# Kernel optimization log

Measured on AMD Instinct MI355X. Metric: run time of the kernel, lower is better.

## Reference

```python
import jax, jax.numpy as jnp
import numpy as np

DIM = 1024
N_HEAD = 16
HEAD_DIM = DIM // N_HEAD
SCALE = HEAD_DIM ** (-0.5)


def setup_inputs() -> dict:
    key = jax.random.key(0)
    ks = jax.random.split(key, 5)
    x = jax.random.normal(ks[0], (2, 2048, DIM), dtype=jnp.float32)
    # Linear params (torch nn.Linear stores weight as [out, in]; we keep [in, out])
    wqkv = jax.random.normal(ks[1], (DIM, 3 * DIM), dtype=jnp.float32) / np.sqrt(DIM)
    bqkv = jax.random.normal(ks[2], (3 * DIM,), dtype=jnp.float32) * 0.01
    wo = jax.random.normal(ks[3], (DIM, DIM), dtype=jnp.float32) / np.sqrt(DIM)
    bo = jax.random.normal(ks[4], (DIM,), dtype=jnp.float32) * 0.01
    return {"x": x, "wqkv": wqkv, "bqkv": bqkv, "wo": wo, "bo": bo}


def reference(x, wqkv, bqkv, wo, bo):
    b, s, _ = x.shape
    qkv = x @ wqkv + bqkv                      # [b, s, 3*dim]
    q, k, v = jnp.split(qkv, 3, axis=-1)
    # [b, s, h, d] -> [b, h, s, d]
    def heads(t):
        return t.reshape(b, s, N_HEAD, HEAD_DIM).transpose(0, 2, 1, 3)
    q, k, v = heads(q) * SCALE, heads(k), heads(v)
    attn = jnp.einsum('bhqd,bhkd->bhqk', q, k)  # [b, h, s, s]
    attn = jax.nn.softmax(attn, axis=-1)
    out = jnp.einsum('bhqk,bhkd->bhqd', attn, v)
    out = out.transpose(0, 2, 1, 3).reshape(b, s, DIM)
    return out @ wo + bo
```

## Files before the change

kernel.cpp:

```cpp
#include <hip/hip_runtime.h>
#include <hip/hip_bf16.h>

#define DIM   1024
#define NHEAD 16
#define HDIM  64
#define BATCH 2
#define SEQ   2048
#define TOK   (BATCH*SEQ)
#define SCALE 0.125f

typedef unsigned short u16;
typedef __attribute__((ext_vector_type(8))) short s16x8;
typedef __attribute__((ext_vector_type(4))) float f32x4;

__device__ __forceinline__ u16 f2bf(float f) {
    union { float f; unsigned u; } v; v.f = f;
    unsigned r = v.u + 0x7fffu + ((v.u >> 16) & 1u);
    return (u16)(r >> 16);
}
__device__ __forceinline__ float bf2f(u16 h) {
    union { unsigned u; float f; } v; v.u = (unsigned)h << 16;
    return v.f;
}
__device__ __forceinline__ unsigned pack2(float a, float b) {
    return (unsigned)f2bf(a) | ((unsigned)f2bf(b) << 16);
}

typedef __attribute__((address_space(3))) void lds_void;
typedef const __attribute__((address_space(1))) void gbl_void;
__device__ __forceinline__ void gload_lds16(const void* g, void* l) {
    __builtin_amdgcn_global_load_lds((gbl_void*)g, (lds_void*)l, 16, 0, 0);
}

__global__ __launch_bounds__(256)
void cvt_bf16(const float* __restrict__ in, u16* __restrict__ out) {
    int i = blockIdx.x * 256 + threadIdx.x;
    float4 v = ((const float4*)in)[i];
    ((uint2*)out)[i] = make_uint2(pack2(v.x, v.y), pack2(v.z, v.w));
}

__global__ __launch_bounds__(256)
void cvt_bf16_T(const float* __restrict__ in, u16* __restrict__ outT,
                int K, int N) {
    __shared__ float t[32][33];
    const int n0 = blockIdx.x * 32, k0 = blockIdx.y * 32;
    const int tx = threadIdx.x & 31, ty = threadIdx.x >> 5;
#pragma unroll
    for (int i = 0; i < 4; ++i)
        t[ty + i * 8][tx] = in[(size_t)(k0 + ty + i * 8) * N + n0 + tx];
    __syncthreads();
#pragma unroll
    for (int i = 0; i < 4; ++i) {
        float v = t[tx][ty + i * 8];
        outT[(size_t)(n0 + ty + i * 8) * K + k0 + tx] = f2bf(v);
    }
}

__global__ __launch_bounds__(256)
void split_cvt_T(const float* __restrict__ in, u16* __restrict__ hiT,
                 u16* __restrict__ loT, int K, int N) {
    __shared__ float t[32][33];
    const int n0 = blockIdx.x * 32, k0 = blockIdx.y * 32;
    const int tx = threadIdx.x & 31, ty = threadIdx.x >> 5;
#pragma unroll
    for (int i = 0; i < 4; ++i)
        t[ty + i * 8][tx] = in[(size_t)(k0 + ty + i * 8) * N + n0 + tx];
    __syncthreads();
#pragma unroll
    for (int i = 0; i < 4; ++i) {
        float v = t[tx][ty + i * 8];
        u16 h = f2bf(v);
        size_t o = (size_t)(n0 + ty + i * 8) * K + k0 + tx;
        hiT[o] = h;
        loT[o] = f2bf(v - bf2f(h));
    }
}

__global__ __launch_bounds__(256)
void gemm_qkv(const u16* __restrict__ Ag, const u16* __restrict__ Bg,
              const float* __restrict__ bias, u16* __restrict__ Qh,
              u16* __restrict__ Kh, u16* __restrict__ Vh, int K, int N) {
    __shared__ u16 As[128 * 64];
    __shared__ u16 Bs[128 * 64];

    const int tid  = threadIdx.x;
    const int lane = tid & 63;
    const int w    = tid >> 6;
    const int c    = lane & 15;
    const int quad = lane >> 4;
    const int wm   = (w & 1) * 64;
    const int wn   = (w >> 1) * 64;
    const int row0 = blockIdx.y * 128;
    const int col0 = blockIdx.x * 128;
    const int sw   = c & 7;

    f32x4 acc[4][4];
#pragma unroll
    for (int m = 0; m < 4; ++m)
#pragma unroll
        for (int n = 0; n < 4; ++n) acc[m][n] = (f32x4){0.f, 0.f, 0.f, 0.f};

    for (int k0 = 0; k0 < K; k0 += 64) {
        __syncthreads();
#pragma unroll
        for (int i = 0; i < 4; ++i) {
            int idx = tid + i * 256;
            int r = idx >> 3, p = idx & 7;
            int g = p ^ (r & 7);
            gload_lds16(Ag + (size_t)(row0 + r) * K + k0 + g * 8, &As[idx * 8]);
            gload_lds16(Bg + (size_t)(col0 + r) * K + k0 + g * 8, &Bs[idx * 8]);
        }
        __syncthreads();

        s16x8 af[4][2];
#pragma unroll
        for (int m = 0; m < 4; ++m)
#pragma unroll
            for (int kh = 0; kh < 2; ++kh)
                af[m][kh] = *(const s16x8*)&As[(wm + m * 16 + c) * 64 +
                                              ((kh * 4 + quad) ^ sw) * 8];
#pragma unroll
        for (int kh = 0; kh < 2; ++kh)
#pragma unroll
            for (int n = 0; n < 4; ++n) {
                s16x8 bf = *(const s16x8*)&Bs[(wn + n * 16 + c) * 64 +
                                              ((kh * 4 + quad) ^ sw) * 8];
#pragma unroll
                for (int m = 0; m < 4; ++m)
                    acc[m][n] = __builtin_amdgcn_mfma_f32_16x16x32_bf16(
                        af[m][kh], bf, acc[m][n], 0, 0, 0);
            }
    }

#pragma unroll
    for (int n = 0; n < 4; ++n) {
        const int col = col0 + wn + n * 16 + c;
        const float bv = bias[col];
        const int h = (col >> 6) & 15, d = col & 63;
#pragma unroll
        for (int m = 0; m < 4; ++m) {
            const int rbase = row0 + wm + m * 16 + quad * 4;
#pragma unroll
            for (int r = 0; r < 4; ++r) {
                const int row = rbase + r;
                const int b = row >> 11, s = row & (SEQ - 1);
                const int bh = (b << 4) + h;
                float v = acc[m][n][r] + bv;
                if (col0 < DIM)
                    Qh[((size_t)bh * SEQ + s) * 64 + d] = f2bf(v * SCALE);
                else if (col0 < 2 * DIM)
                    Kh[((size_t)bh * SEQ + s) * 64 + d] = f2bf(v);
                else
                    Vh[((size_t)bh * 64 + d) * SEQ + s] = f2bf(v);
            }
        }
    }
}

template<int BN_>
__global__ __launch_bounds__(256)
void gemm_bt_split(const u16* __restrict__ Ahg, const u16* __restrict__ Alg,
                   const u16* __restrict__ Bhg, const u16* __restrict__ Blg,
                   const float* __restrict__ bias, float* __restrict__ Cout,
                   int M, int N, int K) {
    constexpr int MT = (BN_ == 128) ? 4 : 2;
    constexpr int NT = 4;
    __shared__ u16 Ah[128 * 32], Al[128 * 32];
    __shared__ u16 Bh[BN_ * 32], Bl[BN_ * 32];

    const int tid  = threadIdx.x;
    const int lane = tid & 63;
    const int w    = tid >> 6;
    const int c    = lane & 15;
    const int quad = lane >> 4;
    const int wm   = (BN_ == 128) ? (w & 1) * 64 : w * 32;
    const int wn   = (BN_ == 128) ? (w >> 1) * 64 : 0;
    const int row0 = blockIdx.y * 128;
    const int col0 = blockIdx.x * BN_;
    const int sw   = (c ^ (c >> 2)) & 3;

    f32x4 acc[MT][NT];
#pragma unroll
    for (int m = 0; m < MT; ++m)
#pragma unroll
        for (int n = 0; n < NT; ++n) acc[m][n] = (f32x4){0.f, 0.f, 0.f, 0.f};

    for (int k0 = 0; k0 < K; k0 += 32) {
        __syncthreads();
#pragma unroll
        for (int i = 0; i < 2; ++i) {
            int idx = tid + i * 256;
            int r = idx >> 2, p = idx & 3;
            int g = p ^ ((r ^ (r >> 2)) & 3);
            size_t so = (size_t)(row0 + r) * K + k0 + g * 8;
            gload_lds16(Ahg + so, &Ah[idx * 8]);
            gload_lds16(Alg + so, &Al[idx * 8]);
        }
#pragma unroll
        for (int i = 0; i < BN_ / 64; ++i) {
            int idx = tid + i * 256;
            int r = idx >> 2, p = idx & 3;
            int g = p ^ ((r ^ (r >> 2)) & 3);
            size_t so = (size_t)(col0 + r) * K + k0 + g * 8;
            gload_lds16(Bhg + so, &Bh[idx * 8]);
            gload_lds16(Blg + so, &Bl[idx * 8]);
        }
        __syncthreads();

        s16x8 ah[MT], al[MT];
#pragma unroll
        for (int m = 0; m < MT; ++m) {
            int ro = (wm + m * 16 + c) * 32 + ((quad ^ sw) * 8);
            ah[m] = *(const s16x8*)&Ah[ro];
            al[m] = *(const s16x8*)&Al[ro];
        }
#pragma unroll
        for (int n = 0; n < NT; ++n) {
            int ro = (wn + n * 16 + c) * 32 + ((quad ^ sw) * 8);
            s16x8 bh = *(const s16x8*)&Bh[ro];
            s16x8 bl = *(const s16x8*)&Bl[ro];
#pragma unroll
            for (int m = 0; m < MT; ++m) {
                acc[m][n] = __builtin_amdgcn_mfma_f32_16x16x32_bf16(ah[m], bh, acc[m][n], 0, 0, 0);
                acc[m][n] = __builtin_amdgcn_mfma_f32_16x16x32_bf16(ah[m], bl, acc[m][n], 0, 0, 0);
                acc[m][n] = __builtin_amdgcn_mfma_f32_16x16x32_bf16(al[m], bh, acc[m][n], 0, 0, 0);
            }
        }
    }

#pragma unroll
    for (int n = 0; n < NT; ++n) {
        const int col = col0 + wn + n * 16 + c;
        const float bv = bias[col];
#pragma unroll
        for (int m = 0; m < MT; ++m) {
            const int rbase = row0 + wm + m * 16 + quad * 4;
#pragma unroll
            for (int r = 0; r < 4; ++r)
                Cout[(size_t)(rbase + r) * N + col] = acc[m][n][r] + bv;
        }
    }
}

__global__ __launch_bounds__(512)
void flash_attn3(const u16* __restrict__ Qg, const u16* __restrict__ Kg,
                 const u16* __restrict__ Vg, u16* __restrict__ out_hi,
                 u16* __restrict__ out_lo) {
    __shared__ u16 Qs[128 * 64];
    __shared__ u16 Ks[2][64 * 64];
    __shared__ u16 Vt[2][64 * 64];
    __shared__ u16 Ps[128][72];

    const int tid  = threadIdx.x;
    const int lane = tid & 63;
    const int ws   = tid >> 6;
    const int c    = lane & 15;
    const int quad = lane >> 4;
    const int ws16 = ws * 16;
    const int bh   = blockIdx.y;
    const int q0   = blockIdx.x * 128;

    const u16* Qb = Qg + (size_t)bh * SEQ * 64;
    const u16* Kb = Kg + (size_t)bh * SEQ * 64;
    const u16* Vb = Vg + (size_t)bh * 64 * SEQ;

    {
#pragma unroll
        for (int i = 0; i < 2; ++i) {
            int idx = tid + i * 512;
            int r = idx >> 3, p = idx & 7, g = p ^ (r & 7);
            gload_lds16(Qb + (size_t)(q0 + r) * 64 + g * 8, &Qs[idx * 8]);
        }
        int r = tid >> 3, p = tid & 7, g = p ^ (r & 7);
        gload_lds16(Kb + (size_t)r * 64 + g * 8, &Ks[0][tid * 8]);
        gload_lds16(Vb + (size_t)r * SEQ + g * 8, &Vt[0][tid * 8]);
    }
    __syncthreads();

    const int sw = c & 7;
    s16x8 aq0 = *(const s16x8*)&Qs[(ws16 + c) * 64 + ((quad ^ sw) * 8)];
    s16x8 aq1 = *(const s16x8*)&Qs[(ws16 + c) * 64 + (((quad | 4) ^ sw) * 8)];

    float l = 0.f;
    f32x4 o[4];
#pragma unroll
    for (int t = 0; t < 4; ++t) o[t] = (f32x4){0.f, 0.f, 0.f, 0.f};

    for (int kt = 0; kt < SEQ / 64; ++kt) {
        const int cur = kt & 1, nxt = cur ^ 1;

        if (kt < SEQ / 64 - 1) {
            const int k1 = (kt + 1) * 64;
            int r = tid >> 3, p = tid & 7, g = p ^ (r & 7);
            gload_lds16(Kb + (size_t)(k1 + r) * 64 + g * 8, &Ks[nxt][tid * 8]);
            gload_lds16(Vb + (size_t)r * SEQ + k1 + g * 8, &Vt[nxt][tid * 8]);
        }

        f32x4 s[4];
#pragma unroll
        for (int t = 0; t < 4; ++t) {
            const int kr = t * 16 + c;
            s16x8 b0 = *(const s16x8*)&Ks[cur][kr * 64 + ((quad ^ sw) * 8)];
            s16x8 b1 = *(const s16x8*)&Ks[cur][kr * 64 + (((quad | 4) ^ sw) * 8)];
            f32x4 z = (f32x4){0.f, 0.f, 0.f, 0.f};
            z = __builtin_amdgcn_mfma_f32_16x16x32_bf16(b0, aq0, z, 0, 0, 0);
            z = __builtin_amdgcn_mfma_f32_16x16x32_bf16(b1, aq1, z, 0, 0, 0);
            s[t] = z;
        }

#pragma unroll
        for (int t = 0; t < 4; ++t) {
            float p0 = __expf(s[t][0]), p1 = __expf(s[t][1]);
            float p2 = __expf(s[t][2]), p3 = __expf(s[t][3]);
            l += (p0 + p1) + (p2 + p3);
            *(uint2*)&Ps[ws16 + c][t * 16 + quad * 4] =
                make_uint2(pack2(p0, p1), pack2(p2, p3));
        }

        s16x8 ap0 = *(const s16x8*)&Ps[ws16 + c][quad * 8];
        s16x8 ap1 = *(const s16x8*)&Ps[ws16 + c][32 + quad * 8];
#pragma unroll
        for (int t = 0; t < 4; ++t) {
            const int vr = t * 16 + c;
            s16x8 b0 = *(const s16x8*)&Vt[cur][vr * 64 + ((quad ^ sw) * 8)];
            s16x8 b1 = *(const s16x8*)&Vt[cur][vr * 64 + (((quad | 4) ^ sw) * 8)];
            o[t] = __builtin_amdgcn_mfma_f32_16x16x32_bf16(ap0, b0, o[t], 0, 0, 0);
            o[t] = __builtin_amdgcn_mfma_f32_16x16x32_bf16(ap1, b1, o[t], 0, 0, 0);
        }

        __syncthreads();
    }

    l += __shfl_xor(l, 16, 64);
    l += __shfl_xor(l, 32, 64);

    const int b = bh >> 4, h = bh & 15;
#pragma unroll
    for (int r = 0; r < 4; ++r) {
        const float lq = __shfl(l, quad * 4 + r, 64);
        const float inv = 1.f / lq;
        const size_t ro = (size_t)(b * SEQ + q0 + ws16 + quad * 4 + r) * DIM + h * HDIM;
#pragma unroll
        for (int t = 0; t < 4; ++t) {
            float of = o[t][r] * inv;
            u16 hv = f2bf(of);
            out_hi[ro + t * 16 + c] = hv;
            out_lo[ro + t * 16 + c] = f2bf(of - bf2f(hv));
        }
    }
}

extern "C" void kernel_launch(void* const* d_in, const int* in_sizes, int n_in,
                              void* d_out, int out_size, void* d_ws, size_t ws_size,
                              hipStream_t stream) {
    (void)in_sizes; (void)n_in; (void)out_size; (void)ws_size;
    const float* x    = (const float*)d_in[0];
    const float* wqkv = (const float*)d_in[1];
    const float* bqkv = (const float*)d_in[2];
    const float* wo   = (const float*)d_in[3];
    const float* bo   = (const float*)d_in[4];
    float* out = (float*)d_out;

    const size_t HB = (size_t)BATCH * NHEAD * SEQ * HDIM;
    u16* Qh  = (u16*)d_ws;
    u16* Kh  = Qh + HB;
    u16* Vh  = Kh + HB;
    u16* ah  = Vh + HB;
    u16* al  = ah + (size_t)TOK * DIM;
    u16* wqT = al + (size_t)TOK * DIM;
    u16* woh = wqT + (size_t)3 * DIM * DIM;
    u16* wol = woh + (size_t)DIM * DIM;
    u16* xb  = wol + (size_t)DIM * DIM;

    cvt_bf16<<<TOK * DIM / 4 / 256, 256, 0, stream>>>(x, xb);
    cvt_bf16_T<<<dim3(3 * DIM / 32, DIM / 32), 256, 0, stream>>>(wqkv, wqT, DIM, 3 * DIM);
    split_cvt_T<<<dim3(DIM / 32, DIM / 32), 256, 0, stream>>>(wo, woh, wol, DIM, DIM);
    gemm_qkv<<<dim3(3 * DIM / 128, TOK / 128), 256, 0, stream>>>(
        xb, wqT, bqkv, Qh, Kh, Vh, DIM, 3 * DIM);
    flash_attn3<<<dim3(SEQ / 128, BATCH * NHEAD), 512, 0, stream>>>(
        Qh, Kh, Vh, ah, al);
    gemm_bt_split<64><<<dim3(DIM / 64, TOK / 128), 256, 0, stream>>>(
        ah, al, woh, wol, bo, out, TOK, DIM, DIM);
}
```

Baseline: 219.9 us.

## Switch pipeline to fp16 and drop split hi/lo output projection

```diff
diff --git a/kernel.cpp b/kernel.cpp
--- a/kernel.cpp
+++ b/kernel.cpp
@@ -7,23 +7,18 @@
 #define BATCH 2
 #define SEQ   2048
 #define TOK   (BATCH*SEQ)
-#define SCALE 0.125f
+#define QSCALE 0.1803368801111204f
 
 typedef unsigned short u16;
-typedef __attribute__((ext_vector_type(8))) short s16x8;
+typedef __attribute__((ext_vector_type(8))) _Float16 h16x8;
 typedef __attribute__((ext_vector_type(4))) float f32x4;
 
-__device__ __forceinline__ u16 f2bf(float f) {
-    union { float f; unsigned u; } v; v.f = f;
-    unsigned r = v.u + 0x7fffu + ((v.u >> 16) & 1u);
-    return (u16)(r >> 16);
-}
-__device__ __forceinline__ float bf2f(u16 h) {
-    union { unsigned u; float f; } v; v.u = (unsigned)h << 16;
-    return v.f;
-}
-__device__ __forceinline__ unsigned pack2(float a, float b) {
-    return (unsigned)f2bf(a) | ((unsigned)f2bf(b) << 16);
+__device__ __forceinline__ u16 f2h(float f) {
+    union { _Float16 h; u16 u; } v; v.h = (_Float16)f;
+    return v.u;
+}
+__device__ __forceinline__ unsigned pack2h(float a, float b) {
+    return (unsigned)f2h(a) | ((unsigned)f2h(b) << 16);
 }
 
 typedef __attribute__((address_space(3))) void lds_void;
@@ -33,15 +28,15 @@
 }
 
 __global__ __launch_bounds__(256)
-void cvt_bf16(const float* __restrict__ in, u16* __restrict__ out) {
+void cvt_f16(const float* __restrict__ in, u16* __restrict__ out) {
     int i = blockIdx.x * 256 + threadIdx.x;
     float4 v = ((const float4*)in)[i];
-    ((uint2*)out)[i] = make_uint2(pack2(v.x, v.y), pack2(v.z, v.w));
+    ((uint2*)out)[i] = make_uint2(pack2h(v.x, v.y), pack2h(v.z, v.w));
 }
 
 __global__ __launch_bounds__(256)
-void cvt_bf16_T(const float* __restrict__ in, u16* __restrict__ outT,
-                int K, int N) {
+void cvt_f16_T(const float* __restrict__ in, u16* __restrict__ outT,
+               int K, int N) {
     __shared__ float t[32][33];
     const int n0 = blockIdx.x * 32, k0 = blockIdx.y * 32;
     const int tx = threadIdx.x & 31, ty = threadIdx.x >> 5;
@@ -50,30 +45,8 @@
         t[ty + i * 8][tx] = in[(size_t)(k0 + ty + i * 8) * N + n0 + tx];
     __syncthreads();
 #pragma unroll
-    for (int i = 0; i < 4; ++i) {
-        float v = t[tx][ty + i * 8];
-        outT[(size_t)(n0 + ty + i * 8) * K + k0 + tx] = f2bf(v);
-    }
-}
-
-__global__ __launch_bounds__(256)
-void split_cvt_T(const float* __restrict__ in, u16* __restrict__ hiT,
-                 u16* __restrict__ loT, int K, int N) {
-    __shared__ float t[32][33];
-    const int n0 = blockIdx.x * 32, k0 = blockIdx.y * 32;
-    const int tx = threadIdx.x & 31, ty = threadIdx.x >> 5;
-#pragma unroll
     for (int i = 0; i < 4; ++i)
-        t[ty + i * 8][tx] = in[(size_t)(k0 + ty + i * 8) * N + n0 + tx];
-    __syncthreads();
-#pragma unroll
-    for (int i = 0; i < 4; ++i) {
-        float v = t[tx][ty + i * 8];
-        u16 h = f2bf(v);
-        size_t o = (size_t)(n0 + ty + i * 8) * K + k0 + tx;
-        hiT[o] = h;
-        loT[o] = f2bf(v - bf2f(h));
-    }
+        outT[(size_t)(n0 + ty + i * 8) * K + k0 + tx] = f2h(t[tx][ty + i * 8]);
 }
 
 __global__ __launch_bounds__(256)
@@ -112,22 +85,22 @@
         }
         __syncthreads();
 
-        s16x8 af[4][2];
+        h16x8 af[4][2];
 #pragma unroll
         for (int m = 0; m < 4; ++m)
 #pragma unroll
             for (int kh = 0; kh < 2; ++kh)
-                af[m][kh] = *(const s16x8*)&As[(wm + m * 16 + c) * 64 +
+                af[m][kh] = *(const h16x8*)&As[(wm + m * 16 + c) * 64 +
                                               ((kh * 4 + quad) ^ sw) * 8];
 #pragma unroll
         for (int kh = 0; kh < 2; ++kh)
 #pragma unroll
             for (int n = 0; n < 4; ++n) {
-                s16x8 bf = *(const s16x8*)&Bs[(wn + n * 16 + c) * 64 +
+                h16x8 bf = *(const h16x8*)&Bs[(wn + n * 16 + c) * 64 +
                                               ((kh * 4 + quad) ^ sw) * 8];
 #pragma unroll
                 for (int m = 0; m < 4; ++m)
-                    acc[m][n] = __builtin_amdgcn_mfma_f32_16x16x32_bf16(
+                    acc[m][n] = __builtin_amdgcn_mfma_f32_16x16x32_f16(
                         af[m][kh], bf, acc[m][n], 0, 0, 0);
             }
     }
@@ -140,100 +113,94 @@
 #pragma unroll
         for (int m = 0; m < 4; ++m) {
             const int rbase = row0 + wm + m * 16 + quad * 4;
-#pragma unroll
-            for (int r = 0; r < 4; ++r) {
-                const int row = rbase + r;
-                const int b = row >> 11, s = row & (SEQ - 1);
-                const int bh = (b << 4) + h;
-                float v = acc[m][n][r] + bv;
-                if (col0 < DIM)
-                    Qh[((size_t)bh * SEQ + s) * 64 + d] = f2bf(v * SCALE);
-                else if (col0 < 2 * DIM)
-                    Kh[((size_t)bh * SEQ + s) * 64 + d] = f2bf(v);
-                else
-                    Vh[((size_t)bh * 64 + d) * SEQ + s] = f2bf(v);
+            const int b = rbase >> 11, s0 = rbase & (SEQ - 1);
+            const int bh = (b << 4) + h;
+            if (col0 < DIM) {
+#pragma unroll
+                for (int r = 0; r < 4; ++r)
+                    Qh[((size_t)bh * SEQ + s0 + r) * 64 + d] =
+                        f2h((acc[m][n][r] + bv) * QSCALE);
+            } else if (col0 < 2 * DIM) {
+#pragma unroll
+                for (int r = 0; r < 4; ++r)
+                    Kh[((size_t)bh * SEQ + s0 + r) * 64 + d] =
+                        f2h(acc[m][n][r] + bv);
+            } else {
+                uint2 pv = make_uint2(pack2h(acc[m][n][0] + bv, acc[m][n][1] + bv),
+                                      pack2h(acc[m][n][2] + bv, acc[m][n][3] + bv));
+                *(uint2*)&Vh[((size_t)bh * 64 + d) * SEQ + s0] = pv;
             }
         }
     }
 }
 
-template<int BN_>
 __global__ __launch_bounds__(256)
-void gemm_bt_split(const u16* __restrict__ Ahg, const u16* __restrict__ Alg,
-                   const u16* __restrict__ Bhg, const u16* __restrict__ Blg,
-                   const float* __restrict__ bias, float* __restrict__ Cout,
-                   int M, int N, int K) {
-    constexpr int MT = (BN_ == 128) ? 4 : 2;
-    constexpr int NT = 4;
-    __shared__ u16 Ah[128 * 32], Al[128 * 32];
-    __shared__ u16 Bh[BN_ * 32], Bl[BN_ * 32];
+void gemm_out(const u16* __restrict__ Ag, const u16* __restrict__ Bg,
+              const float* __restrict__ bias, float* __restrict__ Cout,
+              int M, int N, int K) {
+    __shared__ u16 As[128 * 64];
+    __shared__ u16 Bs[64 * 64];
 
     const int tid  = threadIdx.x;
     const int lane = tid & 63;
     const int w    = tid >> 6;
     const int c    = lane & 15;
     const int quad = lane >> 4;
-    const int wm   = (BN_ == 128) ? (w & 1) * 64 : w * 32;
-    const int wn   = (BN_ == 128) ? (w >> 1) * 64 : 0;
+    const int wm   = w * 32;
     const int row0 = blockIdx.y * 128;
-    const int col0 = blockIdx.x * BN_;
-    const int sw   = (c ^ (c >> 2)) & 3;
-
-    f32x4 acc[MT][NT];
-#pragma unroll
-    for (int m = 0; m < MT; ++m)
-#pragma unroll
-        for (int n = 0; n < NT; ++n) acc[m][n] = (f32x4){0.f, 0.f, 0.f, 0.f};
-
-    for (int k0 = 0; k0 < K; k0 += 32) {
-        __syncthreads();
+    const int col0 = blockIdx.x * 64;
+    const int sw   = c & 7;
+
+    f32x4 acc[2][4];
+#pragma unroll
+    for (int m = 0; m < 2; ++m)
+#pragma unroll
+        for (int n = 0; n < 4; ++n) acc[m][n] = (f32x4){0.f, 0.f, 0.f, 0.f};
+
+    for (int k0 = 0; k0 < K; k0 += 64) {
+        __syncthreads();
+#pragma unroll
+        for (int i = 0; i < 4; ++i) {
+            int idx = tid + i * 256;
+            int r = idx >> 3, p = idx & 7;
+            int g = p ^ (r & 7);
+            gload_lds16(Ag + (size_t)(row0 + r) * K + k0 + g * 8, &As[idx * 8]);
+        }
 #pragma unroll
         for (int i = 0; i < 2; ++i) {
             int idx = tid + i * 256;
-            int r = idx >> 2, p = idx & 3;
-            int g = p ^ ((r ^ (r >> 2)) & 3);
-            size_t so = (size_t)(row0 + r) * K + k0 + g * 8;
-            gload_lds16(Ahg + so, &Ah[idx * 8]);
-            gload_lds16(Alg + so, &Al[idx * 8]);
-        }
-#pragma unroll
-        for (int i = 0; i < BN_ / 64; ++i) {
-            int idx = tid + i * 256;
-            int r = idx >> 2, p = idx & 3;
-            int g = p ^ ((r ^ (r >> 2)) & 3);
-            size_t so = (size_t)(col0 + r) * K + k0 + g * 8;
-            gload_lds16(Bhg + so, &Bh[idx * 8]);
-            gload_lds16(Blg + so, &Bl[idx * 8]);
-        }
-        __syncthreads();
-
-        s16x8 ah[MT], al[MT];
-#pragma unroll
-        for (int m = 0; m < MT; ++m) {
-            int ro = (wm + m * 16 + c) * 32 + ((quad ^ sw) * 8);
-            ah[m] = *(const s16x8*)&Ah[ro];
-            al[m] = *(const s16x8*)&Al[ro];
-        }
-#pragma unroll
-        for (int n = 0; n < NT; ++n) {
-            int ro = (wn + n * 16 + c) * 32 + ((quad ^ sw) * 8);
-            s16x8 bh = *(const s16x8*)&Bh[ro];
-            s16x8 bl = *(const s16x8*)&Bl[ro];
-#pragma unroll
-            for (int m = 0; m < MT; ++m) {
-                acc[m][n] = __builtin_amdgcn_mfma_f32_16x16x32_bf16(ah[m], bh, acc[m][n], 0, 0, 0);
-                acc[m][n] = __builtin_amdgcn_mfma_f32_16x16x32_bf16(ah[m], bl, acc[m][n], 0, 0, 0);
-                acc[m][n] = __builtin_amdgcn_mfma_f32_16x16x32_bf16(al[m], bh, acc[m][n], 0, 0, 0);
+            int r = idx >> 3, p = idx & 7;
+            int g = p ^ (r & 7);
+            gload_lds16(Bg + (size_t)(col0 + r) * K + k0 + g * 8, &Bs[idx * 8]);
+        }
+        __syncthreads();
+
+        h16x8 af[2][2];
+#pragma unroll
+        for (int m = 0; m < 2; ++m)
+#pragma unroll
+            for (int kh = 0; kh < 2; ++kh)
+                af[m][kh] = *(const h16x8*)&As[(wm + m * 16 + c) * 64 +
+                                              ((kh * 4 + quad) ^ sw) * 8];
+#pragma unroll
+        for (int kh = 0; kh < 2; ++kh)
+#pragma unroll
+            for (int n = 0; n < 4; ++n) {
+                h16x8 bf = *(const h16x8*)&Bs[(n * 16 + c) * 64 +
+                                              ((kh * 4 + quad) ^ sw) * 8];
+#pragma unroll
+                for (int m = 0; m < 2; ++m)
+                    acc[m][n] = __builtin_amdgcn_mfma_f32_16x16x32_f16(
+                        af[m][kh], bf, acc[m][n], 0, 0, 0);
             }
-        }
-    }
-
-#pragma unroll
-    for (int n = 0; n < NT; ++n) {
-        const int col = col0 + wn + n * 16 + c;
+    }
+
+#pragma unroll
+    for (int n = 0; n < 4; ++n) {
+        const int col = col0 + n * 16 + c;
         const float bv = bias[col];
 #pragma unroll
-        for (int m = 0; m < MT; ++m) {
+        for (int m = 0; m < 2; ++m) {
             const int rbase = row0 + wm + m * 16 + quad * 4;
 #pragma unroll
             for (int r = 0; r < 4; ++r)
@@ -243,9 +210,8 @@
 }
 
 __global__ __launch_bounds__(512)
-void flash_attn3(const u16* __restrict__ Qg, const u16* __restrict__ Kg,
-                 const u16* __restrict__ Vg, u16* __restrict__ out_hi,
-                 u16* __restrict__ out_lo) {
+void flash_attn4(const u16* __restrict__ Qg, const u16* __restrict__ Kg,
+                 const u16* __restrict__ Vg, u16* __restrict__ aout) {
     __shared__ u16 Qs[128 * 64];
     __shared__ u16 Ks[2][64 * 64];
     __shared__ u16 Vt[2][64 * 64];
@@ -278,8 +244,8 @@
     __syncthreads();
 
     const int sw = c & 7;
-    s16x8 aq0 = *(const s16x8*)&Qs[(ws16 + c) * 64 + ((quad ^ sw) * 8)];
-    s16x8 aq1 = *(const s16x8*)&Qs[(ws16 + c) * 64 + (((quad | 4) ^ sw) * 8)];
+    h16x8 aq0 = *(const h16x8*)&Qs[(ws16 + c) * 64 + ((quad ^ sw) * 8)];
+    h16x8 aq1 = *(const h16x8*)&Qs[(ws16 + c) * 64 + (((quad | 4) ^ sw) * 8)];
 
     float l = 0.f;
     f32x4 o[4];
@@ -300,32 +266,32 @@
 #pragma unroll
         for (int t = 0; t < 4; ++t) {
             const int kr = t * 16 + c;
-            s16x8 b0 = *(const s16x8*)&Ks[cur][kr * 64 + ((quad ^ sw) * 8)];
-            s16x8 b1 = *(const s16x8*)&Ks[cur][kr * 64 + (((quad | 4) ^ sw) * 8)];
+            h16x8 b0 = *(const h16x8*)&Ks[cur][kr * 64 + ((quad ^ sw) * 8)];
+            h16x8 b1 = *(const h16x8*)&Ks[cur][kr * 64 + (((quad | 4) ^ sw) * 8)];
             f32x4 z = (f32x4){0.f, 0.f, 0.f, 0.f};
-            z = __builtin_amdgcn_mfma_f32_16x16x32_bf16(b0, aq0, z, 0, 0, 0);
-            z = __builtin_amdgcn_mfma_f32_16x16x32_bf16(b1, aq1, z, 0, 0, 0);
+            z = __builtin_amdgcn_mfma_f32_16x16x32_f16(b0, aq0, z, 0, 0, 0);
+            z = __builtin_amdgcn_mfma_f32_16x16x32_f16(b1, aq1, z, 0, 0, 0);
             s[t] = z;
         }
 
 #pragma unroll
         for (int t = 0; t < 4; ++t) {
-            float p0 = __expf(s[t][0]), p1 = __expf(s[t][1]);
-            float p2 = __expf(s[t][2]), p3 = __expf(s[t][3]);
+            float p0 = exp2f(s[t][0]), p1 = exp2f(s[t][1]);
+            float p2 = exp2f(s[t][2]), p3 = exp2f(s[t][3]);
             l += (p0 + p1) + (p2 + p3);
             *(uint2*)&Ps[ws16 + c][t * 16 + quad * 4] =
-                make_uint2(pack2(p0, p1), pack2(p2, p3));
-        }
-
-        s16x8 ap0 = *(const s16x8*)&Ps[ws16 + c][quad * 8];
-        s16x8 ap1 = *(const s16x8*)&Ps[ws16 + c][32 + quad * 8];
+                make_uint2(pack2h(p0, p1), pack2h(p2, p3));
+        }
+
+        h16x8 ap0 = *(const h16x8*)&Ps[ws16 + c][quad * 8];
+        h16x8 ap1 = *(const h16x8*)&Ps[ws16 + c][32 + quad * 8];
 #pragma unroll
         for (int t = 0; t < 4; ++t) {
             const int vr = t * 16 + c;
-            s16x8 b0 = *(const s16x8*)&Vt[cur][vr * 64 + ((quad ^ sw) * 8)];
-            s16x8 b1 = *(const s16x8*)&Vt[cur][vr * 64 + (((quad | 4) ^ sw) * 8)];
-            o[t] = __builtin_amdgcn_mfma_f32_16x16x32_bf16(ap0, b0, o[t], 0, 0, 0);
-            o[t] = __builtin_amdgcn_mfma_f32_16x16x32_bf16(ap1, b1, o[t], 0, 0, 0);
+            h16x8 b0 = *(const h16x8*)&Vt[cur][vr * 64 + ((quad ^ sw) * 8)];
+            h16x8 b1 = *(const h16x8*)&Vt[cur][vr * 64 + (((quad | 4) ^ sw) * 8)];
+            o[t] = __builtin_amdgcn_mfma_f32_16x16x32_f16(ap0, b0, o[t], 0, 0, 0);
+            o[t] = __builtin_amdgcn_mfma_f32_16x16x32_f16(ap1, b1, o[t], 0, 0, 0);
         }
 
         __syncthreads();
@@ -341,12 +307,8 @@
         const float inv = 1.f / lq;
         const size_t ro = (size_t)(b * SEQ + q0 + ws16 + quad * 4 + r) * DIM + h * HDIM;
 #pragma unroll
-        for (int t = 0; t < 4; ++t) {
-            float of = o[t][r] * inv;
-            u16 hv = f2bf(of);
-            out_hi[ro + t * 16 + c] = hv;
-            out_lo[ro + t * 16 + c] = f2bf(of - bf2f(hv));
-        }
+        for (int t = 0; t < 4; ++t)
+            aout[ro + t * 16 + c] = f2h(o[t][r] * inv);
     }
 }
 
@@ -365,20 +327,18 @@
     u16* Qh  = (u16*)d_ws;
     u16* Kh  = Qh + HB;
     u16* Vh  = Kh + HB;
-    u16* ah  = Vh + HB;
-    u16* al  = ah + (size_t)TOK * DIM;
-    u16* wqT = al + (size_t)TOK * DIM;
-    u16* woh = wqT + (size_t)3 * DIM * DIM;
-    u16* wol = woh + (size_t)DIM * DIM;
-    u16* xb  = wol + (size_t)DIM * DIM;
-
-    cvt_bf16<<<TOK * DIM / 4 / 256, 256, 0, stream>>>(x, xb);
-    cvt_bf16_T<<<dim3(3 * DIM / 32, DIM / 32), 256, 0, stream>>>(wqkv, wqT, DIM, 3 * DIM);
-    split_cvt_T<<<dim3(DIM / 32, DIM / 32), 256, 0, stream>>>(wo, woh, wol, DIM, DIM);
+    u16* ao  = Vh + HB;
+    u16* wqT = ao + (size_t)TOK * DIM;
+    u16* woT = wqT + (size_t)3 * DIM * DIM;
+    u16* xh  = woT + (size_t)DIM * DIM;
+
+    cvt_f16<<<TOK * DIM / 4 / 256, 256, 0, stream>>>(x, xh);
+    cvt_f16_T<<<dim3(3 * DIM / 32, DIM / 32), 256, 0, stream>>>(wqkv, wqT, DIM, 3 * DIM);
+    cvt_f16_T<<<dim3(DIM / 32, DIM / 32), 256, 0, stream>>>(wo, woT, DIM, DIM);
     gemm_qkv<<<dim3(3 * DIM / 128, TOK / 128), 256, 0, stream>>>(
-        xb, wqT, bqkv, Qh, Kh, Vh, DIM, 3 * DIM);
-    flash_attn3<<<dim3(SEQ / 128, BATCH * NHEAD), 512, 0, stream>>>(
-        Qh, Kh, Vh, ah, al);
-    gemm_bt_split<64><<<dim3(DIM / 64, TOK / 128), 256, 0, stream>>>(
-        ah, al, woh, wol, bo, out, TOK, DIM, DIM);
-}
+        xh, wqT, bqkv, Qh, Kh, Vh, DIM, 3 * DIM);
+    flash_attn4<<<dim3(SEQ / 128, BATCH * NHEAD), 512, 0, stream>>>(
+        Qh, Kh, Vh, ao);
+    gemm_out<<<dim3(DIM / 64, TOK / 128), 256, 0, stream>>>(
+        ao, woT, bo, out, TOK, DIM, DIM);
+}
```

Result: faster. 199.3 us (-9.4%).
